# Kernel optimization log

Hardware: AMD Instinct MI355X
Metric: run time of the kernel (lower is better)

## Reference

```python
import jax, jax.numpy as jnp
import numpy as np
from jax import lax

B, P, W, C = 32, 256, 16, 64
H = 128          # hidden_dim
PRED = 64        # pred_stat_len
TOK = W + 1      # token_len
SIGMA_MIN = 1e-3
EPS = 1e-5


def setup_inputs() -> dict:
    key = jax.random.key(0)
    ks = jax.random.split(key, 20)
    s = 0.05
    inp = {
        "mu_hist": jax.random.normal(ks[0], (B, P, C), jnp.float32),
        "std_hist": jax.random.uniform(ks[1], (B, P, C), jnp.float32, 0.1, 1.5),
        "anchor": jax.random.normal(ks[2], (B, 1, C), jnp.float32),
        "raw_patches": jax.random.normal(ks[3], (B, P, W, C), jnp.float32),
        # mean branch params
        "mean_in_W": jax.random.normal(ks[4], (TOK, H), jnp.float32) * s,
        "mean_in_b": jax.random.normal(ks[5], (H,), jnp.float32) * s,
        "mean_a_logit": jnp.full((H,), float(np.log(9.0)), jnp.float32),
        "mean_post_W": jax.random.normal(ks[6], (H, H), jnp.float32) * s,
        "mean_post_b": jax.random.normal(ks[7], (H,), jnp.float32) * s,
        "mean_out_W": jax.random.normal(ks[8], (H, PRED), jnp.float32) * s,
        "mean_out_b": jax.random.normal(ks[9], (PRED,), jnp.float32) * s,
        "gamma_mu": jax.random.normal(ks[10], (C,), jnp.float32) * s,
        # std branch params
        "std_in_W": jax.random.normal(ks[11], (TOK, H), jnp.float32) * s,
        "std_in_b": jax.random.normal(ks[12], (H,), jnp.float32) * s,
        "std_a_logit": jnp.full((H,), float(np.log(9.0)), jnp.float32),
        "std_post_W": jax.random.normal(ks[13], (H, H), jnp.float32) * s,
        "std_post_b": jax.random.normal(ks[14], (H,), jnp.float32) * s,
        "std_out_W": jax.random.normal(ks[15], (H, PRED), jnp.float32) * s,
        "std_out_b": jax.random.normal(ks[16], (PRED,), jnp.float32) * s,
        "gamma_std": jax.random.normal(ks[17], (C,), jnp.float32) * s,
    }
    return inp


def _ema(u, a_logit):
    # u: (BC, P, H) -> final hidden state (BC, H) via h_t = a*h + (1-a)*u_t
    a = jax.nn.sigmoid(a_logit)
    one_minus_a = 1.0 - a

    def step(h, u_t):
        return a * h + one_minus_a * u_t, None

    h0 = jnp.zeros((u.shape[0], u.shape[2]), u.dtype)
    h, _ = lax.scan(step, h0, jnp.swapaxes(u, 0, 1))  # scan over P
    return h


def _branch(token, in_W, in_b, a_logit, post_W, post_b, out_W, out_b):
    u = token @ in_W + in_b                     # (BC, P, H)
    h = _ema(u, a_logit)                        # (BC, H)
    h = h + jax.nn.gelu(h, approximate=False) @ post_W + post_b
    res = h @ out_W + out_b                     # (BC, PRED)
    return res.reshape(B, C, PRED).transpose(0, 2, 1)  # (B, PRED, C)


def reference(mu_hist, std_hist, anchor, raw_patches,
              mean_in_W, mean_in_b, mean_a_logit, mean_post_W, mean_post_b,
              mean_out_W, mean_out_b, gamma_mu,
              std_in_W, std_in_b, std_a_logit, std_post_W, std_post_b,
              std_out_W, std_out_b, gamma_std):
    BC = B * C
    # --- mean branch ---
    mu_center = mu_hist - anchor                                 # (B,P,C)
    raw_center = raw_patches - anchor[:, :, None, :]             # (B,P,W,C)
    mu_center_t = mu_center.transpose(0, 2, 1).reshape(BC, P, 1)
    raw_center_t = raw_center.transpose(0, 3, 1, 2).reshape(BC, P, W)
    mean_token = jnp.concatenate([mu_center_t, raw_center_t], axis=-1)
    mu_res = _branch(mean_token, mean_in_W, mean_in_b, mean_a_logit,
                     mean_post_W, mean_post_b, mean_out_W, mean_out_b)
    mu_fut = anchor + gamma_mu[None, None, :] * mu_res           # (B,PRED,C)

    # --- std branch ---
    logstd_hist = jnp.log(jnp.maximum(std_hist, SIGMA_MIN))      # (B,P,C)
    logstd_anchor = logstd_hist.mean(axis=1, keepdims=True)      # (B,1,C)
    logstd_center = logstd_hist - logstd_anchor
    z_patch = (raw_patches - mu_hist[:, :, None, :]) / (std_hist[:, :, None, :] + EPS)
    logstd_center_t = logstd_center.transpose(0, 2, 1).reshape(BC, P, 1)
    z_patch_t = z_patch.transpose(0, 3, 1, 2).reshape(BC, P, W)
    std_token = jnp.concatenate([logstd_center_t, z_patch_t], axis=-1)
    logstd_res = _branch(std_token, std_in_W, std_in_b, std_a_logit,
                         std_post_W, std_post_b, std_out_W, std_out_b)
    logstd_fut = logstd_anchor + gamma_std[None, None, :] * logstd_res
    std_fut = jnp.maximum(jnp.exp(logstd_fut), SIGMA_MIN)
    return mu_fut, std_fut
```

## Files before the change

kernel.cpp:

```cpp
#include <hip/hip_runtime.h>
#include <math.h>

#define Bn 32
#define Pn 256
#define Wn 16
#define Cn 64
#define Hn 128
#define PREDn 64
#define TOKn 17
#define TBLK 8

__global__ void lsa_part_kernel(const float* __restrict__ std_hist,
                                float* __restrict__ lsa_part) {
  int b = blockIdx.x;
  int ts = blockIdx.y;
  int c = threadIdx.x & 63;
  int q = threadIdx.x >> 6;
  const float* base = std_hist + ((size_t)b * Pn + ts * 32) * Cn + c;
  float s = 0.f;
#pragma unroll
  for (int i = 0; i < 8; ++i) {
    int t = q + 4 * i;
    s += logf(fmaxf(base[(size_t)t * Cn], 1e-3f));
  }
  __shared__ float red[4][64];
  red[q][c] = s;
  __syncthreads();
  if (q == 0) {
    lsa_part[ts * 2048 + b * 64 + c] = red[0][c] + red[1][c] + red[2][c] + red[3][c];
  }
}

__global__ void lsa_combine_kernel(const float* __restrict__ lsa_part,
                                   float* __restrict__ lsa) {
  int i = blockIdx.x * 256 + threadIdx.x;
  float v = 0.f;
#pragma unroll
  for (int k = 0; k < 8; ++k) v += lsa_part[k * 2048 + i];
  lsa[i] = v * (1.0f / 256.0f);
}

template <int NCH>
__launch_bounds__(256, 2)
__global__ void ema_kernel(
    const float* __restrict__ mu_hist, const float* __restrict__ std_hist,
    const float* __restrict__ raw,
    const float* __restrict__ mW, const float* __restrict__ mb, const float* __restrict__ mal,
    const float* __restrict__ sW, const float* __restrict__ sb, const float* __restrict__ sal,
    float* __restrict__ Spart) {
  constexpr int L = Pn / NCH;
  constexpr int NPH = L / TBLK;
  const int sx = blockIdx.x;
  const int cblk = sx & 1, hblk = (sx >> 1) & 1, ph = sx >> 2;
  const int b = blockIdx.y, br = blockIdx.z;
  const int tid = threadIdx.x;
  const int cr = tid & 31;
  const int w0 = tid >> 5;

  const float* inW = br ? sW : mW;
  const float* inb = br ? sb : mb;
  const float* alog = br ? sal : mal;
  const int hh0 = hblk * 64 + w0 * 8;
  const int rot = (cr >> 3) & 3;

  float Wr[TOKn][8];
#pragma unroll
  for (int j = 0; j < 16; ++j) {
    int feat = 1 + 4 * (((j >> 2) + 4 - rot) & 3) + (j & 3);
    float4 wv0 = *(const float4*)&inW[feat * Hn + hh0];
    float4 wv1 = *(const float4*)&inW[feat * Hn + hh0 + 4];
    Wr[j][0] = wv0.x; Wr[j][1] = wv0.y; Wr[j][2] = wv0.z; Wr[j][3] = wv0.w;
    Wr[j][4] = wv1.x; Wr[j][5] = wv1.y; Wr[j][6] = wv1.z; Wr[j][7] = wv1.w;
  }
  {
    float4 wv0 = *(const float4*)&inW[hh0];
    float4 wv1 = *(const float4*)&inW[hh0 + 4];
    Wr[16][0] = wv0.x; Wr[16][1] = wv0.y; Wr[16][2] = wv0.z; Wr[16][3] = wv0.w;
    Wr[16][4] = wv1.x; Wr[16][5] = wv1.y; Wr[16][6] = wv1.z; Wr[16][7] = wv1.w;
  }
  float av[8], bias[8], h[8];
#pragma unroll
  for (int i = 0; i < 8; ++i) {
    av[i] = 1.0f / (1.0f + expf(-alog[hh0 + i]));
    bias[i] = inb[hh0 + i];
    h[i] = 0.0f;
  }

  const int cs = cblk * 32 + cr;
  const size_t bP = (size_t)b * Pn;
  const float* rawb = raw + bP * Wn * Cn;
  const float* mub = mu_hist + bP * Cn;
  const float* stdb = std_hist + bP * Cn;

  __shared__ float tok[2][TBLK][32 * 20];

  const int wf1 = cr * 20 + 4 * (((w0 >> 2) + rot) & 3) + (w0 & 3);
  const int wf2 = cr * 20 + 4 * ((((w0 + 8) >> 2) + rot) & 3) + (w0 & 3);
  const int cmu = tid & 31;
  const int tqmu = tid >> 5;
  const int wq_s = cmu * 20 + 16 + ((cmu >> 3) & 3);
  const int cmug = cblk * 32 + cmu;
  const int qo = cr * 20 + 16 + rot;

  const int t0 = ph * L;

  auto STAGE = [&](int tb, int buf) {
#pragma unroll
    for (int tq = 0; tq < TBLK; ++tq) {
      int t = tb + tq;
      const float* rawt = rawb + (size_t)t * (Wn * Cn);
      float r0 = rawt[w0 * Cn + cs];
      float r1 = rawt[(w0 + 8) * Cn + cs];
      if (br == 0) {
        tok[buf][tq][wf1] = r0;
        tok[buf][tq][wf2] = r1;
      } else {
        float mu = mub[(size_t)t * Cn + cs];
        float sd = stdb[(size_t)t * Cn + cs];
        float inv = 1.0f / (sd + 1e-5f);
        tok[buf][tq][wf1] = (r0 - mu) * inv;
        tok[buf][tq][wf2] = (r1 - mu) * inv;
      }
    }
    {
      int t = tb + tqmu;
      float v = br ? logf(fmaxf(stdb[(size_t)t * Cn + cmug], 1e-3f))
                   : mub[(size_t)t * Cn + cmug];
      tok[buf][tqmu][wq_s] = v;
    }
  };

  auto COMPUTE = [&](int buf) {
#pragma unroll
    for (int tq = 0; tq < TBLK; ++tq) {
      const float* row = &tok[buf][tq][cr * 20];
      float4 q0 = *(const float4*)(row);
      float4 q1 = *(const float4*)(row + 4);
      float4 q2 = *(const float4*)(row + 8);
      float4 q3 = *(const float4*)(row + 12);
      float q4 = tok[buf][tq][qo];
#pragma unroll
      for (int i = 0; i < 8; ++i) {
        float u = bias[i];
        u = fmaf(q0.x, Wr[0][i], u);
        u = fmaf(q0.y, Wr[1][i], u);
        u = fmaf(q0.z, Wr[2][i], u);
        u = fmaf(q0.w, Wr[3][i], u);
        u = fmaf(q1.x, Wr[4][i], u);
        u = fmaf(q1.y, Wr[5][i], u);
        u = fmaf(q1.z, Wr[6][i], u);
        u = fmaf(q1.w, Wr[7][i], u);
        u = fmaf(q2.x, Wr[8][i], u);
        u = fmaf(q2.y, Wr[9][i], u);
        u = fmaf(q2.z, Wr[10][i], u);
        u = fmaf(q2.w, Wr[11][i], u);
        u = fmaf(q3.x, Wr[12][i], u);
        u = fmaf(q3.y, Wr[13][i], u);
        u = fmaf(q3.z, Wr[14][i], u);
        u = fmaf(q3.w, Wr[15][i], u);
        u = fmaf(q4, Wr[16][i], u);
        h[i] = fmaf(av[i], h[i] - u, u);
      }
    }
  };

  STAGE(t0, 0);
  __syncthreads();
  int cur = 0;
#pragma unroll 1
  for (int p = 0; p < NPH; ++p) {
    if (p + 1 < NPH) STAGE(t0 + (p + 1) * TBLK, cur ^ 1);
    COMPUTE(cur);
    __syncthreads();
    cur ^= 1;
  }

  const int idx_block = (((br * NCH + ph) * Bn + b) * 2 + cblk) * 2 + hblk;
  float* op = Spart + (size_t)idx_block * 2048 + tid * 8;
  float4 o0 = {h[0], h[1], h[2], h[3]};
  float4 o1 = {h[4], h[5], h[6], h[7]};
  *(float4*)op = o0;
  *(float4*)(op + 4) = o1;
}

template <int G, int NCH>
__launch_bounds__(128, 4)
__global__ void head_kernel(
    const float* __restrict__ anchor, const float* __restrict__ lsa,
    const float* __restrict__ mW, const float* __restrict__ sW,
    const float* __restrict__ mal, const float* __restrict__ mpW, const float* __restrict__ mpb,
    const float* __restrict__ moW, const float* __restrict__ mob, const float* __restrict__ gmu,
    const float* __restrict__ sal, const float* __restrict__ spW, const float* __restrict__ spb,
    const float* __restrict__ soW, const float* __restrict__ sob, const float* __restrict__ gst,
    const float* __restrict__ Spart, float* __restrict__ out) {
  constexpr int L = Pn / NCH;
  const int br = blockIdx.y;
  const int bc0 = blockIdx.x * G;
  const int tid = threadIdx.x;
  const float* alog = br ? sal : mal;
  const float* pW = br ? spW : mpW;
  const float* pb = br ? spb : mpb;
  const float* oW = br ? soW : moW;
  const float* ob = br ? sob : mob;

  __shared__ float smem[2 * G * 128];
  float* g_lds = smem;
  float* h2 = smem + G * 128;

  const float a = 1.0f / (1.0f + expf(-alog[tid]));
  float aL = a;
#pragma unroll
  for (int s7 = 0; s7 < 31 - __builtin_clz(L); ++s7) aL *= aL;
  float fac[NCH];
  fac[NCH - 1] = 1.0f;
#pragma unroll
  for (int k = NCH - 2; k >= 0; --k) fac[k] = fac[k + 1] * aL;
  const float apF = fac[0] * aL;
  float SWv;
  if (br == 0) {
    float s = 0.f;
#pragma unroll
    for (int k = 0; k < TOKn; ++k) s += mW[k * Hn + tid];
    SWv = s;
  } else {
    SWv = sW[tid];
  }
  const float cS = (1.0f - apF) * SWv;

  const int hblk = tid >> 6;
  const int hhg = (tid >> 3) & 7;
  const int ii = tid & 7;

  float hreg[G];
#pragma unroll
  for (int g = 0; g < G; ++g) {
    int bc = bc0 + g;
    int bb = bc >> 6, cc = bc & 63;
    int cblk2 = cc >> 5, crr = cc & 31;
    const size_t inner = (size_t)(hhg * 32 + crr) * 8 + ii;
    const int blk0 = (((br * NCH + 0) * Bn + bb) * 2 + cblk2) * 2 + hblk;
    float hv = 0.f;
#pragma unroll
    for (int k = 0; k < NCH; ++k) {
      hv = fmaf(fac[k], Spart[(size_t)(blk0 + k * (Bn * 4)) * 2048 + inner], hv);
    }
    float shiftv = br ? lsa[bb * Cn + cc] : anchor[bb * Cn + cc];
    hv = fmaf(-cS, shiftv, hv);
    hreg[g] = hv;
    g_lds[g * 128 + tid] = 0.5f * hv * (1.0f + erff(hv * 0.70710678118654752f));
  }
  __syncthreads();

  float acc[G];
#pragma unroll
  for (int g = 0; g < G; ++g) acc[g] = hreg[g] + pb[tid];
  for (int j = 0; j < 128; j += 4) {
    float w0v = pW[j * Hn + tid];
    float w1v = pW[(j + 1) * Hn + tid];
    float w2v = pW[(j + 2) * Hn + tid];
    float w3v = pW[(j + 3) * Hn + tid];
#pragma unroll
    for (int g = 0; g < G; ++g) {
      float4 gv = *(const float4*)&g_lds[g * 128 + j];
      acc[g] = fmaf(gv.x, w0v, acc[g]);
      acc[g] = fmaf(gv.y, w1v, acc[g]);
      acc[g] = fmaf(gv.z, w2v, acc[g]);
      acc[g] = fmaf(gv.w, w3v, acc[g]);
    }
  }
#pragma unroll
  for (int g = 0; g < G; ++g) h2[g * 128 + tid] = acc[g];
  __syncthreads();

  const int p = tid & 63;
  const int jh = tid >> 6;
  float s[G];
#pragma unroll
  for (int g = 0; g < G; ++g) s[g] = 0.f;
  for (int jj = 0; jj < 64; jj += 4) {
    int j = jh * 64 + jj;
    float w0v = oW[j * PREDn + p];
    float w1v = oW[(j + 1) * PREDn + p];
    float w2v = oW[(j + 2) * PREDn + p];
    float w3v = oW[(j + 3) * PREDn + p];
#pragma unroll
    for (int g = 0; g < G; ++g) {
      float4 hv4 = *(const float4*)&h2[g * 128 + j];
      s[g] = fmaf(hv4.x, w0v, s[g]);
      s[g] = fmaf(hv4.y, w1v, s[g]);
      s[g] = fmaf(hv4.z, w2v, s[g]);
      s[g] = fmaf(hv4.w, w3v, s[g]);
    }
  }
  float* red = smem;
#pragma unroll
  for (int g = 0; g < G; ++g) red[jh * (G * 64) + g * 64 + p] = s[g];
  __syncthreads();
  if (tid < 64) {
#pragma unroll
    for (int g = 0; g < G; ++g) {
      int bc = bc0 + g;
      int bb = bc >> 6, cc = bc & 63;
      float tot = red[g * 64 + p] + red[G * 64 + g * 64 + p] + ob[p];
      if (br == 0) {
        out[((size_t)bb * PREDn + p) * Cn + cc] = fmaf(gmu[cc], tot, anchor[bb * Cn + cc]);
      } else {
        float lf = fmaf(gst[cc], tot, lsa[bb * Cn + cc]);
        out[131072 + ((size_t)bb * PREDn + p) * Cn + cc] = fmaxf(expf(lf), 1e-3f);
      }
    }
  }
}

extern "C" void kernel_launch(void* const* d_in, const int* in_sizes, int n_in,
                              void* d_out, int out_size, void* d_ws, size_t ws_size,
                              hipStream_t stream) {
  (void)in_sizes; (void)n_in; (void)out_size;
  const float* mu_hist = (const float*)d_in[0];
  const float* std_hist = (const float*)d_in[1];
  const float* anchor = (const float*)d_in[2];
  const float* raw = (const float*)d_in[3];
  const float* mW = (const float*)d_in[4];
  const float* mb_ = (const float*)d_in[5];
  const float* mal = (const float*)d_in[6];
  const float* mpW = (const float*)d_in[7];
  const float* mpb = (const float*)d_in[8];
  const float* moW = (const float*)d_in[9];
  const float* mob = (const float*)d_in[10];
  const float* gmu = (const float*)d_in[11];
  const float* sW = (const float*)d_in[12];
  const float* sb_ = (const float*)d_in[13];
  const float* sal = (const float*)d_in[14];
  const float* spW = (const float*)d_in[15];
  const float* spb = (const float*)d_in[16];
  const float* soW = (const float*)d_in[17];
  const float* sob = (const float*)d_in[18];
  const float* gst = (const float*)d_in[19];
  float* out = (float*)d_out;
  float* ws = (float*)d_ws;

  float* lsa = ws;
  float* lsa_part = ws + 2048;
  float* Spart = ws + 2048 + 16384;

  const size_t need4 = (size_t)(2048 + 16384 + 1024 * 2048) * 4;

  hipLaunchKernelGGL(lsa_part_kernel, dim3(32, 8), dim3(256), 0, stream, std_hist, lsa_part);
  hipLaunchKernelGGL(lsa_combine_kernel, dim3(8), dim3(256), 0, stream, lsa_part, lsa);
  if (ws_size >= need4) {
    hipLaunchKernelGGL(HIP_KERNEL_NAME(ema_kernel<4>), dim3(16, 32, 2), dim3(256), 0, stream,
                       mu_hist, std_hist, raw, mW, mb_, mal, sW, sb_, sal, Spart);
    hipLaunchKernelGGL(HIP_KERNEL_NAME(head_kernel<2, 4>), dim3(1024, 2), dim3(128), 0, stream,
                       anchor, lsa, mW, sW, mal, mpW, mpb, moW, mob, gmu,
                       sal, spW, spb, soW, sob, gst, Spart, out);
  } else {
    hipLaunchKernelGGL(HIP_KERNEL_NAME(ema_kernel<2>), dim3(8, 32, 2), dim3(256), 0, stream,
                       mu_hist, std_hist, raw, mW, mb_, mal, sW, sb_, sal, Spart);
    hipLaunchKernelGGL(HIP_KERNEL_NAME(head_kernel<2, 2>), dim3(1024, 2), dim3(128), 0, stream,
                       anchor, lsa, mW, sW, mal, mpW, mpb, moW, mob, gmu,
                       sal, spW, spb, soW, sob, gst, Spart, out);
  }
}
```

Baseline: 212.4 us.

## Stage EMA tokens via direct global-to-LDS loads and fold normalization algebraically

```diff
diff --git a/kernel.cpp b/kernel.cpp
--- a/kernel.cpp
+++ b/kernel.cpp
@@ -10,6 +10,12 @@
 #define TOKn 17
 #define TBLK 8
 
+__device__ __forceinline__ void gload_lds(const float* g, float* l) {
+  __builtin_amdgcn_global_load_lds(
+      (const __attribute__((address_space(1))) unsigned int*)g,
+      (__attribute__((address_space(3))) unsigned int*)l, 4, 0, 0);
+}
+
 __global__ void lsa_part_kernel(const float* __restrict__ std_hist,
                                 float* __restrict__ lsa_part) {
   int b = blockIdx.x;
@@ -45,8 +51,8 @@
 __global__ void ema_kernel(
     const float* __restrict__ mu_hist, const float* __restrict__ std_hist,
     const float* __restrict__ raw,
-    const float* __restrict__ mW, const float* __restrict__ mb, const float* __restrict__ mal,
-    const float* __restrict__ sW, const float* __restrict__ sb, const float* __restrict__ sal,
+    const float* __restrict__ mW, const float* __restrict__ mal,
+    const float* __restrict__ sW, const float* __restrict__ sal,
     float* __restrict__ Spart) {
   constexpr int L = Pn / NCH;
   constexpr int NPH = L / TBLK;
@@ -58,118 +64,105 @@
   const int w0 = tid >> 5;
 
   const float* inW = br ? sW : mW;
-  const float* inb = br ? sb : mb;
   const float* alog = br ? sal : mal;
   const int hh0 = hblk * 64 + w0 * 8;
-  const int rot = (cr >> 3) & 3;
 
   float Wr[TOKn][8];
 #pragma unroll
-  for (int j = 0; j < 16; ++j) {
-    int feat = 1 + 4 * (((j >> 2) + 4 - rot) & 3) + (j & 3);
-    float4 wv0 = *(const float4*)&inW[feat * Hn + hh0];
-    float4 wv1 = *(const float4*)&inW[feat * Hn + hh0 + 4];
-    Wr[j][0] = wv0.x; Wr[j][1] = wv0.y; Wr[j][2] = wv0.z; Wr[j][3] = wv0.w;
-    Wr[j][4] = wv1.x; Wr[j][5] = wv1.y; Wr[j][6] = wv1.z; Wr[j][7] = wv1.w;
+  for (int k = 0; k < 16; ++k) {
+    float4 a0 = *(const float4*)&inW[(1 + k) * Hn + hh0];
+    float4 a1 = *(const float4*)&inW[(1 + k) * Hn + hh0 + 4];
+    Wr[k][0] = a0.x; Wr[k][1] = a0.y; Wr[k][2] = a0.z; Wr[k][3] = a0.w;
+    Wr[k][4] = a1.x; Wr[k][5] = a1.y; Wr[k][6] = a1.z; Wr[k][7] = a1.w;
   }
   {
-    float4 wv0 = *(const float4*)&inW[hh0];
-    float4 wv1 = *(const float4*)&inW[hh0 + 4];
-    Wr[16][0] = wv0.x; Wr[16][1] = wv0.y; Wr[16][2] = wv0.z; Wr[16][3] = wv0.w;
-    Wr[16][4] = wv1.x; Wr[16][5] = wv1.y; Wr[16][6] = wv1.z; Wr[16][7] = wv1.w;
-  }
-  float av[8], bias[8], h[8];
+    float4 a0 = *(const float4*)&inW[hh0];
+    float4 a1 = *(const float4*)&inW[hh0 + 4];
+    Wr[16][0] = a0.x; Wr[16][1] = a0.y; Wr[16][2] = a0.z; Wr[16][3] = a0.w;
+    Wr[16][4] = a1.x; Wr[16][5] = a1.y; Wr[16][6] = a1.z; Wr[16][7] = a1.w;
+  }
+  float SW[8], av[8], h[8];
 #pragma unroll
   for (int i = 0; i < 8; ++i) {
+    float s = 0.f;
+#pragma unroll
+    for (int k = 0; k < 16; ++k) s += Wr[k][i];
+    SW[i] = s;
     av[i] = 1.0f / (1.0f + expf(-alog[hh0 + i]));
-    bias[i] = inb[hh0 + i];
     h[i] = 0.0f;
   }
 
-  const int cs = cblk * 32 + cr;
-  const size_t bP = (size_t)b * Pn;
-  const float* rawb = raw + bP * Wn * Cn;
-  const float* mub = mu_hist + bP * Cn;
-  const float* stdb = std_hist + bP * Cn;
-
-  __shared__ float tok[2][TBLK][32 * 20];
-
-  const int wf1 = cr * 20 + 4 * (((w0 >> 2) + rot) & 3) + (w0 & 3);
-  const int wf2 = cr * 20 + 4 * ((((w0 + 8) >> 2) + rot) & 3) + (w0 & 3);
-  const int cmu = tid & 31;
-  const int tqmu = tid >> 5;
-  const int wq_s = cmu * 20 + 16 + ((cmu >> 3) & 3);
-  const int cmug = cblk * 32 + cmu;
-  const int qo = cr * 20 + 16 + rot;
-
+  const int chalf = cblk * 32;
+  const float* rawb = raw + ((size_t)b * Pn) * (Wn * Cn) + chalf;
+  const float* mub = mu_hist + ((size_t)b * Pn) * Cn + chalf;
+  const float* sdb = std_hist + ((size_t)b * Pn) * Cn + chalf;
+
+  __shared__ float tokf[2][TBLK][16][32];
+  __shared__ float mu_l[2][TBLK][32];
+  __shared__ float sd_l[2][TBLK][32];
+
+  const int lane = tid & 63;
+  const int wv = tid >> 6;
+  const int lw = lane >> 5;
+  const int lc = lane & 31;
+  const int r0 = wv * 2;
   const int t0 = ph * L;
 
-  auto STAGE = [&](int tb, int buf) {
-#pragma unroll
-    for (int tq = 0; tq < TBLK; ++tq) {
-      int t = tb + tq;
-      const float* rawt = rawb + (size_t)t * (Wn * Cn);
-      float r0 = rawt[w0 * Cn + cs];
-      float r1 = rawt[(w0 + 8) * Cn + cs];
+  auto ISSUE = [&](int tb, int buf) {
+#pragma unroll
+    for (int rr = 0; rr < 2; ++rr) {
+      const int row = r0 + rr;
+      const float* gb = rawb + (size_t)(tb + row) * (Wn * Cn);
+#pragma unroll
+      for (int k = 0; k < 16; k += 2) {
+        gload_lds(gb + (k + lw) * Cn + lc, &tokf[buf][row][k][0]);
+      }
+    }
+    gload_lds(mub + (size_t)(tb + r0 + lw) * Cn + lc, &mu_l[buf][r0][0]);
+    if (br) gload_lds(sdb + (size_t)(tb + r0 + lw) * Cn + lc, &sd_l[buf][r0][0]);
+  };
+
+  auto COMPUTE = [&](int buf) {
+#pragma unroll
+    for (int r = 0; r < TBLK; ++r) {
+      float tk[16];
+#pragma unroll
+      for (int k = 0; k < 16; ++k) tk[k] = tokf[buf][r][k][cr];
+      float sc = mu_l[buf][r][cr];
       if (br == 0) {
-        tok[buf][tq][wf1] = r0;
-        tok[buf][tq][wf2] = r1;
+#pragma unroll
+        for (int i = 0; i < 8; ++i) {
+          float u = tk[0] * Wr[0][i];
+#pragma unroll
+          for (int k = 1; k < 16; ++k) u = fmaf(tk[k], Wr[k][i], u);
+          u = fmaf(sc, Wr[16][i], u);
+          h[i] = fmaf(av[i], h[i] - u, u);
+        }
       } else {
-        float mu = mub[(size_t)t * Cn + cs];
-        float sd = stdb[(size_t)t * Cn + cs];
+        float sd = sd_l[buf][r][cr];
         float inv = 1.0f / (sd + 1e-5f);
-        tok[buf][tq][wf1] = (r0 - mu) * inv;
-        tok[buf][tq][wf2] = (r1 - mu) * inv;
+        float ls = logf(fmaxf(sd, 1e-3f));
+        float nmi = -sc * inv;
+#pragma unroll
+        for (int i = 0; i < 8; ++i) {
+          float u = tk[0] * Wr[0][i];
+#pragma unroll
+          for (int k = 1; k < 16; ++k) u = fmaf(tk[k], Wr[k][i], u);
+          u = u * inv;
+          u = fmaf(nmi, SW[i], u);
+          u = fmaf(ls, Wr[16][i], u);
+          h[i] = fmaf(av[i], h[i] - u, u);
+        }
       }
     }
-    {
-      int t = tb + tqmu;
-      float v = br ? logf(fmaxf(stdb[(size_t)t * Cn + cmug], 1e-3f))
-                   : mub[(size_t)t * Cn + cmug];
-      tok[buf][tqmu][wq_s] = v;
-    }
   };
 
-  auto COMPUTE = [&](int buf) {
-#pragma unroll
-    for (int tq = 0; tq < TBLK; ++tq) {
-      const float* row = &tok[buf][tq][cr * 20];
-      float4 q0 = *(const float4*)(row);
-      float4 q1 = *(const float4*)(row + 4);
-      float4 q2 = *(const float4*)(row + 8);
-      float4 q3 = *(const float4*)(row + 12);
-      float q4 = tok[buf][tq][qo];
-#pragma unroll
-      for (int i = 0; i < 8; ++i) {
-        float u = bias[i];
-        u = fmaf(q0.x, Wr[0][i], u);
-        u = fmaf(q0.y, Wr[1][i], u);
-        u = fmaf(q0.z, Wr[2][i], u);
-        u = fmaf(q0.w, Wr[3][i], u);
-        u = fmaf(q1.x, Wr[4][i], u);
-        u = fmaf(q1.y, Wr[5][i], u);
-        u = fmaf(q1.z, Wr[6][i], u);
-        u = fmaf(q1.w, Wr[7][i], u);
-        u = fmaf(q2.x, Wr[8][i], u);
-        u = fmaf(q2.y, Wr[9][i], u);
-        u = fmaf(q2.z, Wr[10][i], u);
-        u = fmaf(q2.w, Wr[11][i], u);
-        u = fmaf(q3.x, Wr[12][i], u);
-        u = fmaf(q3.y, Wr[13][i], u);
-        u = fmaf(q3.z, Wr[14][i], u);
-        u = fmaf(q3.w, Wr[15][i], u);
-        u = fmaf(q4, Wr[16][i], u);
-        h[i] = fmaf(av[i], h[i] - u, u);
-      }
-    }
-  };
-
-  STAGE(t0, 0);
+  ISSUE(t0, 0);
   __syncthreads();
   int cur = 0;
 #pragma unroll 1
   for (int p = 0; p < NPH; ++p) {
-    if (p + 1 < NPH) STAGE(t0 + (p + 1) * TBLK, cur ^ 1);
+    if (p + 1 < NPH) ISSUE(t0 + (p + 1) * TBLK, cur ^ 1);
     COMPUTE(cur);
     __syncthreads();
     cur ^= 1;
@@ -188,6 +181,7 @@
 __global__ void head_kernel(
     const float* __restrict__ anchor, const float* __restrict__ lsa,
     const float* __restrict__ mW, const float* __restrict__ sW,
+    const float* __restrict__ mIB, const float* __restrict__ sIB,
     const float* __restrict__ mal, const float* __restrict__ mpW, const float* __restrict__ mpb,
     const float* __restrict__ moW, const float* __restrict__ mob, const float* __restrict__ gmu,
     const float* __restrict__ sal, const float* __restrict__ spW, const float* __restrict__ spb,
@@ -202,6 +196,7 @@
   const float* pb = br ? spb : mpb;
   const float* oW = br ? soW : moW;
   const float* ob = br ? sob : mob;
+  const float inb = br ? sIB[tid] : mIB[tid];
 
   __shared__ float smem[2 * G * 128];
   float* g_lds = smem;
@@ -225,7 +220,8 @@
   } else {
     SWv = sW[tid];
   }
-  const float cS = (1.0f - apF) * SWv;
+  const float om = 1.0f - apF;
+  const float cS = om * SWv;
 
   const int hblk = tid >> 6;
   const int hhg = (tid >> 3) & 7;
@@ -246,6 +242,7 @@
     }
     float shiftv = br ? lsa[bb * Cn + cc] : anchor[bb * Cn + cc];
     hv = fmaf(-cS, shiftv, hv);
+    hv = fmaf(om, inb, hv);
     hreg[g] = hv;
     g_lds[g * 128 + tid] = 0.5f * hv * (1.0f + erff(hv * 0.70710678118654752f));
   }
@@ -349,15 +346,15 @@
   hipLaunchKernelGGL(lsa_combine_kernel, dim3(8), dim3(256), 0, stream, lsa_part, lsa);
   if (ws_size >= need4) {
     hipLaunchKernelGGL(HIP_KERNEL_NAME(ema_kernel<4>), dim3(16, 32, 2), dim3(256), 0, stream,
-                       mu_hist, std_hist, raw, mW, mb_, mal, sW, sb_, sal, Spart);
+                       mu_hist, std_hist, raw, mW, mal, sW, sal, Spart);
     hipLaunchKernelGGL(HIP_KERNEL_NAME(head_kernel<2, 4>), dim3(1024, 2), dim3(128), 0, stream,
-                       anchor, lsa, mW, sW, mal, mpW, mpb, moW, mob, gmu,
+                       anchor, lsa, mW, sW, mb_, sb_, mal, mpW, mpb, moW, mob, gmu,
                        sal, spW, spb, soW, sob, gst, Spart, out);
   } else {
     hipLaunchKernelGGL(HIP_KERNEL_NAME(ema_kernel<2>), dim3(8, 32, 2), dim3(256), 0, stream,
-                       mu_hist, std_hist, raw, mW, mb_, mal, sW, sb_, sal, Spart);
+                       mu_hist, std_hist, raw, mW, mal, sW, sal, Spart);
     hipLaunchKernelGGL(HIP_KERNEL_NAME(head_kernel<2, 2>), dim3(1024, 2), dim3(128), 0, stream,
-                       anchor, lsa, mW, sW, mal, mpW, mpb, moW, mob, gmu,
+                       anchor, lsa, mW, sW, mb_, sb_, mal, mpW, mpb, moW, mob, gmu,
                        sal, spW, spb, soW, sob, gst, Spart, out);
   }
 }
```

After: 221.6 us. 4.3% more time.
